# Kernel optimization log

Measured on AMD Instinct MI355X. Metric: run time of the kernel, lower is better.

Reference implementation:

```python
import jax, jax.numpy as jnp
import numpy as np

B, N0, NCLS = 8, 1024, 40
SPACING, SIGMA_FACTOR = 2.0, 1.0
BLOCKS = [[64, 64], [128, 128], [256, 1024]]
POOL_SIZES = [256, 64, 1]
FC1, FC2 = 512, 256
# 3x3x3 kernel translation grid (27-point support, hard-coded in ConvLayer)
GRID = jnp.asarray(np.array([[i, j, k] for i in (-1, 0, 1) for j in (-1, 0, 1) for k in (-1, 0, 1)], dtype=np.float32))  # [27,3]


def pcnn_conv(pc, feat, W, b, sigma):
    """Extension-operator point convolution.
    pc [B,N,3], feat [B,N,Cin], W [27,Cin,Cout], b [Cout].
    out[b,i,o] = relu( (1/N) * sum_l sum_j exp(-||p_i - p_j + t_l||^2/(2 ks^2)) f[b,j] @ W[l] + b )
    """
    ks = SIGMA_FACTOR * sigma
    trans = SPACING * sigma * GRID                      # [27,3]
    inv = 1.0 / (2.0 * ks * ks)
    diff = pc[:, :, None, :] - pc[:, None, :, :]        # [B,N,N,3]
    d2 = jnp.sum(diff * diff, -1)                       # [B,N,N]
    n = pc.shape[1]

    def body(acc, wt):
        t, Wl = wt                                      # t [3], Wl [Cin,Cout]
        # ||diff + t||^2 = d2 + 2 diff.t + |t|^2
        e = jnp.exp(-(d2 + 2.0 * jnp.einsum('bijd,d->bij', diff, t) + jnp.dot(t, t)) * inv)
        s = jnp.einsum('bij,bjc->bic', e, feat)         # Gaussian-weighted gather
        return acc + jnp.einsum('bic,co->bio', s, Wl), None

    out0 = jnp.zeros((pc.shape[0], n, W.shape[2]), feat.dtype)
    out, _ = jax.lax.scan(body, out0, (trans, W))
    return jax.nn.relu(out / n + b)


def fps(pts, m):
    """Farthest point sampling. pts [N,3] -> indices [m]."""
    d = jnp.sum((pts - pts[0]) ** 2, -1)
    idxs = jnp.zeros((m,), jnp.int32)

    def body(i, state):
        idxs, d = state
        nxt = jnp.argmax(d).astype(jnp.int32)
        idxs = idxs.at[i].set(nxt)
        d = jnp.minimum(d, jnp.sum((pts - pts[nxt]) ** 2, -1))
        return idxs, d

    idxs, _ = jax.lax.fori_loop(1, m, body, (idxs, d))
    return idxs


def pool(pc, feat, m):
    """FPS subsample to m centers, max-pool features over nearest-center clusters."""
    idx = jax.vmap(lambda p: fps(p, m))(pc)                      # [B,m]
    centers = jnp.take_along_axis(pc, idx[..., None], axis=1)    # [B,m,3]
    dist = jnp.sum((pc[:, :, None, :] - centers[:, None, :, :]) ** 2, -1)  # [B,N,m]
    assign = jnp.argmin(dist, -1)                                # [B,N]
    pooled = jax.vmap(lambda f, a: jax.ops.segment_max(f, a, num_segments=m))(feat, assign)
    return centers, pooled


def bn(x, g, b):
    mu = jnp.mean(x, 0)
    v = jnp.var(x, 0)
    return g * (x - mu) * jax.lax.rsqrt(v + 1e-5) + b


def setup_inputs() -> dict:
    key = jax.random.key(0)
    ks = jax.random.split(key, 24)
    inp = {"pc": jax.random.normal(ks[0], (B, 3, N0), jnp.float32)}
    chans = [4, 64, 64, 128, 128, 256, 1024]
    for i, (ci, co) in enumerate(zip(chans[:-1], chans[1:])):
        inp[f"w_c{i}"] = jax.random.normal(ks[1 + i], (27, ci, co), jnp.float32) * 0.05
        inp[f"b_c{i}"] = jnp.zeros((co,), jnp.float32)
    inp["w_fc1"] = jax.random.normal(ks[10], (1024, FC1), jnp.float32) * 0.03
    inp["g_fc1"] = jnp.ones((FC1,), jnp.float32)
    inp["be_fc1"] = jnp.zeros((FC1,), jnp.float32)
    inp["w_fc2"] = jax.random.normal(ks[11], (FC1, FC2), jnp.float32) * 0.05
    inp["g_fc2"] = jnp.ones((FC2,), jnp.float32)
    inp["be_fc2"] = jnp.zeros((FC2,), jnp.float32)
    inp["w_fc3"] = jax.random.normal(ks[12], (FC2, NCLS), jnp.float32) * 0.05
    inp["b_fc3"] = jnp.zeros((NCLS,), jnp.float32)
    return inp


def reference(pc, w_c0, b_c0, w_c1, b_c1, w_c2, b_c2, w_c3, b_c3, w_c4, b_c4, w_c5, b_c5,
              w_fc1, g_fc1, be_fc1, w_fc2, g_fc2, be_fc2, w_fc3, b_fc3):
    pts = jnp.transpose(pc, (0, 2, 1))                           # [B,N,3]
    b_, n0, _ = pts.shape
    feat = jnp.concatenate([pts, jnp.ones((b_, n0, 1), pts.dtype)], -1)  # [B,N,4]
    sigma = 1.0 / float(np.sqrt(n0))  # faithfully uses initial N for all blocks
    ws = [(w_c0, b_c0), (w_c1, b_c1), (w_c2, b_c2), (w_c3, b_c3), (w_c4, b_c4), (w_c5, b_c5)]
    idx = 0
    cur = pts
    for bi, block in enumerate(BLOCKS):
        for _ in block:
            W, bb = ws[idx]
            feat = pcnn_conv(cur, feat, W, bb, sigma)
            idx += 1
        cur, feat = pool(cur, feat, POOL_SIZES[bi])
    x = feat.reshape(b_, -1)                                     # [B,1024]
    x = jax.nn.relu(bn(x @ w_fc1, g_fc1, be_fc1))
    x = jax.nn.relu(bn(x @ w_fc2, g_fc2, be_fc2))
    return x @ w_fc3 + b_fc3
```

## Files before the change

### kernel.cpp

```cpp
#include <hip/hip_runtime.h>
#include <cstdint>
#include <cstddef>
#include <cmath>

constexpr int B = 8;
constexpr int N0 = 1024;
constexpr int CAP = 64;
using u16 = unsigned short;

typedef __bf16 bf16x8 __attribute__((ext_vector_type(8)));
typedef float f32x4 __attribute__((ext_vector_type(4)));

__device__ inline u16 f2bf(float x) {
  unsigned u = __float_as_uint(x);
  return (u16)((u + 0x7fffu + ((u >> 16) & 1u)) >> 16);
}
__device__ inline float bf2f(u16 h) { return __uint_as_float(((unsigned)h) << 16); }
__device__ inline int swk2(int row, int k) {
  int s = (((row >> 2) ^ (row >> 4)) & 3);
  return ((((k >> 3) ^ s) << 3) | (k & 7));
}

__global__ __launch_bounds__(256) void k_prep(const float* __restrict__ pc,
                                              float* __restrict__ pts,
                                              float* __restrict__ feat0,
                                              uint4* __restrict__ p3, int n3,
                                              uint4* __restrict__ p6, int n6,
                                              uint4* __restrict__ p9, int n9) {
  int idx = blockIdx.x * blockDim.x + threadIdx.x;
  if (idx < B * N0) {
    int b = idx / N0, i = idx - b * N0;
    float x = pc[(b * 3 + 0) * N0 + i];
    float y = pc[(b * 3 + 1) * N0 + i];
    float z = pc[(b * 3 + 2) * N0 + i];
    pts[idx * 3 + 0] = x; pts[idx * 3 + 1] = y; pts[idx * 3 + 2] = z;
    feat0[idx * 4 + 0] = x; feat0[idx * 4 + 1] = y; feat0[idx * 4 + 2] = z; feat0[idx * 4 + 3] = 1.0f;
  }
  uint4 v = make_uint4(0xFFFFFFFFu, 0xFFFFFFFFu, 0xFFFFFFFFu, 0xFFFFFFFFu);
  for (int i = idx; i < n3; i += B * N0) p3[i] = v;
  for (int i = idx; i < n6; i += B * N0) p6[i] = v;
  for (int i = idx; i < n9; i += B * N0) p9[i] = v;
}

__global__ __launch_bounds__(256) void k_pairs(const float* __restrict__ pts,
                                               int* __restrict__ pidx, int* __restrict__ pcnt,
                                               int N) {
  const int r = blockIdx.x * 4 + (threadIdx.x >> 6);
  const int lane = threadIdx.x & 63;
  const int b = r / N;
  const float px = pts[(size_t)r * 3 + 0];
  const float py = pts[(size_t)r * 3 + 1];
  const float pz = pts[(size_t)r * 3 + 2];
  int* row = pidx + (size_t)r * CAP;
  int base = 0;
  for (int j0 = 0; j0 < N; j0 += 64) {
    int j = j0 + lane;
    float dx = px - pts[((size_t)b * N + j) * 3 + 0];
    float dy = py - pts[((size_t)b * N + j) * 3 + 1];
    float dz = pz - pts[((size_t)b * N + j) * 3 + 2];
    float d2 = dx * dx + dy * dy + dz * dz;
    bool keep = d2 <= 0.1228f;
    unsigned long long mk = __ballot(keep);
    int pos = __popcll(mk & ((1ull << lane) - 1ull));
    if (keep) { int s = base + pos; if (s < CAP) row[s] = j; }
    base += __popcll(mk);
  }
  if (lane == 0) pcnt[r] = base < CAP ? base : CAP;
}

__device__ __forceinline__ void econ_dev(float (*eL)[28],
                                         const float* __restrict__ pts,
                                         const float* __restrict__ feat,
                                         const int* __restrict__ pidx,
                                         const int* __restrict__ pcnt,
                                         u16* __restrict__ Shi, u16* __restrict__ Slo,
                                         int N, int Cin, int K, int Kpad, int mbase,
                                         int blockX) {
  const int g = mbase + blockX;
  const int b = g / N;
  const int t = threadIdx.x;
  const int w = t >> 6, lane = t & 63;
  const bool cact = t < Cin;
  const float px = pts[(size_t)g * 3 + 0];
  const float py = pts[(size_t)g * 3 + 1];
  const float pz = pts[(size_t)g * 3 + 2];
  float sxc = 0.f, syc = 0.f, szc = 0.f, cst = 0.f;
  if (lane < 27) {
    int a = lane / 9, bb = (lane / 3) % 3, cc = lane % 3;
    sxc = (a == 0) ? 64.f : ((a == 2) ? -64.f : 0.f);
    syc = (bb == 0) ? 64.f : ((bb == 2) ? -64.f : 0.f);
    szc = (cc == 0) ? 64.f : ((cc == 2) ? -64.f : 0.f);
    cst = -2.f * (float)((a != 1) + (bb != 1) + (cc != 1));
  }
  float acc[27];
#pragma unroll
  for (int l = 0; l < 27; ++l) acc[l] = 0.f;
  const int n = pcnt[g];
  const int* row = pidx + (size_t)g * CAP;
  for (int p = 0; p < n; ++p) {
    int j = row[p];
    size_t jb = (size_t)b * N + j;
    float dx = px - pts[jb * 3 + 0];
    float dy = py - pts[jb * 3 + 1];
    float dz = pz - pts[jb * 3 + 2];
    float d2 = dx * dx + dy * dy + dz * dz;
    if (lane < 27) {
      float ex = fmaf(-512.f, d2, fmaf(sxc, dx, fmaf(syc, dy, fmaf(szc, dz, cst))));
      eL[w][lane] = __expf(ex);
    }
    asm volatile("s_waitcnt lgkmcnt(0)" ::: "memory");
    __builtin_amdgcn_sched_barrier(0);
    float fv = cact ? feat[jb * Cin + t] : 0.f;
#pragma unroll
    for (int l = 0; l < 27; ++l) acc[l] = fmaf(eL[w][l], fv, acc[l]);
  }
  size_t rowo = (size_t)blockX * Kpad;
  if (cact) {
#pragma unroll
    for (int l = 0; l < 27; ++l) {
      float v = acc[l];
      u16 h = f2bf(v);
      u16 lo = f2bf(v - bf2f(h));
      Shi[rowo + (size_t)l * Cin + t] = h;
      Slo[rowo + (size_t)l * Cin + t] = lo;
    }
  }
  if (Kpad > K && t >= Cin && t < Cin + (Kpad - K)) {
    size_t po = rowo + K + (t - Cin);
    Shi[po] = 0; Slo[po] = 0;
  }
}

__global__ void k_econtract(const float* __restrict__ pts, const float* __restrict__ feat,
                            const int* __restrict__ pidx, const int* __restrict__ pcnt,
                            u16* __restrict__ Shi, u16* __restrict__ Slo,
                            int N, int Cin, int K, int Kpad, int mbase) {
  __shared__ float eL[4][28];
  econ_dev(eL, pts, feat, pidx, pcnt, Shi, Slo, N, Cin, K, Kpad, mbase, blockIdx.x);
}

template <int CTRL>
__device__ __forceinline__ float dppmaxf(float v) {
  int o = __builtin_amdgcn_update_dpp(0, __float_as_int(v), CTRL, 0xF, 0xF, true);
  return fmaxf(v, __int_as_float(o));
}
__device__ __forceinline__ float wavemaxf(float v) {
  v = dppmaxf<0xB1>(v);
  v = dppmaxf<0x4E>(v);
  v = dppmaxf<0x141>(v);
  v = dppmaxf<0x140>(v);
  v = dppmaxf<0x142>(v);
  v = dppmaxf<0x143>(v);
  return __uint_as_float((unsigned)__builtin_amdgcn_readlane(__float_as_int(v), 63));
}

#define FPS_LOAD(i) \
  float qx##i = src[3 * i + 0], qy##i = src[3 * i + 1], qz##i = src[3 * i + 2];
#define FPS_PIN(i) \
  asm volatile("" : "+v"(qx##i), "+v"(qy##i), "+v"(qz##i));
#define FPS_D0A(i) \
  { float ax = __fsub_rn(qx##i, x0), ay = __fsub_rn(qy##i, y0), az = __fsub_rn(qz##i, z0); \
    d##i = __fadd_rn(__fadd_rn(__fmul_rn(ax, ax), __fmul_rn(ay, ay)), __fmul_rn(az, az)); }
#define FPS_UPD(i) \
  { float ax = __fsub_rn(qx##i, cx), ay = __fsub_rn(qy##i, cy), az = __fsub_rn(qz##i, cz); \
    float nd = __fadd_rn(__fadd_rn(__fmul_rn(ax, ax), __fmul_rn(ay, ay)), __fmul_rn(az, az)); \
    d##i = fminf(d##i, nd); }
#define FPS_SEL(i) \
  { bool e = (d##i == lbest); sx = e ? qx##i : sx; sy = e ? qy##i : sy; sz = e ? qz##i : sz; }

__device__ __noinline__ void fps1024_dev(const float* __restrict__ P,
                                         float* __restrict__ centers, int m, int b, int t,
                                         int it0, int it1, float* __restrict__ Dst) {
  const float* src = P + t * 48;
  FPS_LOAD(0) FPS_LOAD(1) FPS_LOAD(2) FPS_LOAD(3)
  FPS_LOAD(4) FPS_LOAD(5) FPS_LOAD(6) FPS_LOAD(7)
  FPS_LOAD(8) FPS_LOAD(9) FPS_LOAD(10) FPS_LOAD(11)
  FPS_LOAD(12) FPS_LOAD(13) FPS_LOAD(14) FPS_LOAD(15)
  FPS_PIN(0) FPS_PIN(1) FPS_PIN(2) FPS_PIN(3)
  FPS_PIN(4) FPS_PIN(5) FPS_PIN(6) FPS_PIN(7)
  FPS_PIN(8) FPS_PIN(9) FPS_PIN(10) FPS_PIN(11)
  FPS_PIN(12) FPS_PIN(13) FPS_PIN(14) FPS_PIN(15)
  float d0, d1, d2, d3, d4, d5, d6, d7, d8, d9, d10, d11, d12, d13, d14, d15;
  if (it0 == 1) {
    float x0 = P[0], y0 = P[1], z0 = P[2];
    FPS_D0A(0) FPS_D0A(1) FPS_D0A(2) FPS_D0A(3)
    FPS_D0A(4) FPS_D0A(5) FPS_D0A(6) FPS_D0A(7)
    FPS_D0A(8) FPS_D0A(9) FPS_D0A(10) FPS_D0A(11)
    FPS_D0A(12) FPS_D0A(13) FPS_D0A(14) FPS_D0A(15)
    if (t == 0) {
      centers[(size_t)b * m * 3 + 0] = x0;
      centers[(size_t)b * m * 3 + 1] = y0;
      centers[(size_t)b * m * 3 + 2] = z0;
    }
  } else {
    const float* ds = Dst + t * 16;
    d0 = ds[0]; d1 = ds[1]; d2 = ds[2]; d3 = ds[3];
    d4 = ds[4]; d5 = ds[5]; d6 = ds[6]; d7 = ds[7];
    d8 = ds[8]; d9 = ds[9]; d10 = ds[10]; d11 = ds[11];
    d12 = ds[12]; d13 = ds[13]; d14 = ds[14]; d15 = ds[15];
  }
  for (int it = it0; it < it1; ++it) {
    float lbest;
    {
      float a0 = fmaxf(d0, d1), a1 = fmaxf(d2, d3), a2 = fmaxf(d4, d5), a3 = fmaxf(d6, d7);
      float a4 = fmaxf(d8, d9), a5 = fmaxf(d10, d11), a6 = fmaxf(d12, d13), a7 = fmaxf(d14, d15);
      float b0 = fmaxf(a0, a1), b1 = fmaxf(a2, a3), b2 = fmaxf(a4, a5), b3 = fmaxf(a6, a7);
      lbest = fmaxf(fmaxf(b0, b1), fmaxf(b2, b3));
    }
    float sx = qx15, sy = qy15, sz = qz15;
    FPS_SEL(14) FPS_SEL(13) FPS_SEL(12) FPS_SEL(11)
    FPS_SEL(10) FPS_SEL(9) FPS_SEL(8) FPS_SEL(7)
    FPS_SEL(6) FPS_SEL(5) FPS_SEL(4) FPS_SEL(3)
    FPS_SEL(2) FPS_SEL(1) FPS_SEL(0)
    float wmax = wavemaxf(lbest);
    unsigned long long mask = __ballot(lbest == wmax);
    int fl = __ffsll((long long)mask) - 1;
    float cx = __uint_as_float((unsigned)__builtin_amdgcn_readlane(__float_as_int(sx), fl));
    float cy = __uint_as_float((unsigned)__builtin_amdgcn_readlane(__float_as_int(sy), fl));
    float cz = __uint_as_float((unsigned)__builtin_amdgcn_readlane(__float_as_int(sz), fl));
    if (t == 0) {
      centers[((size_t)b * m + it) * 3 + 0] = cx;
      centers[((size_t)b * m + it) * 3 + 1] = cy;
      centers[((size_t)b * m + it) * 3 + 2] = cz;
    }
    FPS_UPD(0) FPS_UPD(1) FPS_UPD(2) FPS_UPD(3)
    FPS_UPD(4) FPS_UPD(5) FPS_UPD(6) FPS_UPD(7)
    FPS_UPD(8) FPS_UPD(9) FPS_UPD(10) FPS_UPD(11)
    FPS_UPD(12) FPS_UPD(13) FPS_UPD(14) FPS_UPD(15)
  }
  if (it1 < m) {
    float* ds = Dst + t * 16;
    ds[0] = d0; ds[1] = d1; ds[2] = d2; ds[3] = d3;
    ds[4] = d4; ds[5] = d5; ds[6] = d6; ds[7] = d7;
    ds[8] = d8; ds[9] = d9; ds[10] = d10; ds[11] = d11;
    ds[12] = d12; ds[13] = d13; ds[14] = d14; ds[15] = d15;
  }
}

__device__ __noinline__ void fps256_dev(const float* __restrict__ P,
                                        float* __restrict__ centers, int m, int b, int t,
                                        int it0, int it1, float* __restrict__ Dst) {
  const float* src = P + t * 12;
  FPS_LOAD(0) FPS_LOAD(1) FPS_LOAD(2) FPS_LOAD(3)
  FPS_PIN(0) FPS_PIN(1) FPS_PIN(2) FPS_PIN(3)
  float d0, d1, d2, d3;
  if (it0 == 1) {
    float x0 = P[0], y0 = P[1], z0 = P[2];
    FPS_D0A(0) FPS_D0A(1) FPS_D0A(2) FPS_D0A(3)
    if (t == 0) {
      centers[(size_t)b * m * 3 + 0] = x0;
      centers[(size_t)b * m * 3 + 1] = y0;
      centers[(size_t)b * m * 3 + 2] = z0;
    }
  } else {
    const float* ds = Dst + t * 4;
    d0 = ds[0]; d1 = ds[1]; d2 = ds[2]; d3 = ds[3];
  }
  for (int it = it0; it < it1; ++it) {
    float lbest = fmaxf(fmaxf(d0, d1), fmaxf(d2, d3));
    float sx = qx3, sy = qy3, sz = qz3;
    FPS_SEL(2) FPS_SEL(1) FPS_SEL(0)
    float wmax = wavemaxf(lbest);
    unsigned long long mask = __ballot(lbest == wmax);
    int fl = __ffsll((long long)mask) - 1;
    float cx = __uint_as_float((unsigned)__builtin_amdgcn_readlane(__float_as_int(sx), fl));
    float cy = __uint_as_float((unsigned)__builtin_amdgcn_readlane(__float_as_int(sy), fl));
    float cz = __uint_as_float((unsigned)__builtin_amdgcn_readlane(__float_as_int(sz), fl));
    if (t == 0) {
      centers[((size_t)b * m + it) * 3 + 0] = cx;
      centers[((size_t)b * m + it) * 3 + 1] = cy;
      centers[((size_t)b * m + it) * 3 + 2] = cz;
    }
    FPS_UPD(0) FPS_UPD(1) FPS_UPD(2) FPS_UPD(3)
  }
  if (it1 < m) {
    float* ds = Dst + t * 4;
    ds[0] = d0; ds[1] = d1; ds[2] = d2; ds[3] = d3;
  }
}

__global__ __launch_bounds__(64, 1) void k_econtract_fps(
    const float* __restrict__ pts, const float* __restrict__ feat,
    const int* __restrict__ pidx, const int* __restrict__ pcnt,
    u16* __restrict__ Shi, u16* __restrict__ Slo,
    int N, int Cin, int K, int Kpad, int mbase,
    int fpsMode, const float* __restrict__ fpsPts, float* __restrict__ fpsCenters, int fpsM,
    int it0, int it1, float* __restrict__ fpsD) {
  __shared__ float eL[4][28];
  const int nEcon = gridDim.x - B;
  if ((int)blockIdx.x >= nEcon) {
    const int b = blockIdx.x - nEcon;
    const int t = threadIdx.x;
    if (fpsMode == 1) fps1024_dev(fpsPts + (size_t)b * 1024 * 3, fpsCenters, fpsM, b, t,
                                  it0, it1, fpsD + (size_t)b * 1024);
    else fps256_dev(fpsPts + (size_t)b * 256 * 3, fpsCenters, fpsM, b, t,
                    it0, it1, fpsD + (size_t)b * 256);
    return;
  }
  econ_dev(eL, pts, feat, pidx, pcnt, Shi, Slo, N, Cin, K, Kpad, mbase, blockIdx.x);
}

__global__ __launch_bounds__(512) void k_gemm_mfma(const u16* __restrict__ Shi,
                                                   const u16* __restrict__ Slo,
                                                   const float* __restrict__ W,
                                                   const float* __restrict__ bias,
                                                   float* __restrict__ out,
                                                   float* __restrict__ P,
                                                   int K, int Kpad, int Cout, float scale,
                                                   int mcur) {
  __shared__ u16 As[2][2][32][40];
  __shared__ u16 Bs[2][2][64][40];
  __shared__ float xch[4][64][8];
  const int t = threadIdx.x;
  const int h = t >> 8;
  const int tl = t & 255;
  const int nb = blockIdx.x * 64;
  const int m0 = blockIdx.y * 32;
  const int l = t & 63, w = t >> 6;
  const int ks = w >> 2, wq = w & 3;
  const int wm = (wq >> 1) * 16, wn = (wq & 1) * 32;
  const int la = l & 15, lg = l >> 4;
  const int ntiles = Kpad >> 6;
  const int KZ = gridDim.z, z = blockIdx.z;
  const int q = ntiles / KZ, r = ntiles % KZ;
  const int t0 = z * q + (z < r ? z : r);
  const int cnt = q + (z < r ? 1 : 0);
  const int ar = tl >> 3, ak = (tl & 7) * 4;
  const size_t aOff = (size_t)(m0 + ar) * Kpad + h * 32 + ak;
  const int aw = swk2(ar, ak);
  const int kp = (tl >> 4) * 2, n4 = (tl & 15) * 4;
  f32x4 acc0 = {0.f, 0.f, 0.f, 0.f}, acc1 = {0.f, 0.f, 0.f, 0.f};

  for (int kt = 0; kt < cnt; ++kt) {
    const int k0 = (t0 + kt) * 64;
    *(ushort4*)&As[h][0][ar][aw] = *(const ushort4*)(Shi + aOff + k0);
    *(ushort4*)&As[h][1][ar][aw] = *(const ushort4*)(Slo + aOff + k0);
    {
      int gk0 = k0 + h * 32 + kp;
      float4 b0 = make_float4(0.f, 0.f, 0.f, 0.f), b1 = b0;
      if (gk0 < K) b0 = *(const float4*)(W + (size_t)gk0 * Cout + nb + n4);
      if (gk0 + 1 < K) b1 = *(const float4*)(W + (size_t)(gk0 + 1) * Cout + nb + n4);
      float v0[4] = {b0.x, b0.y, b0.z, b0.w};
      float v1[4] = {b1.x, b1.y, b1.z, b1.w};
#pragma unroll
      for (int e = 0; e < 4; ++e) {
        int n = n4 + e;
        int kw = swk2(n, kp);
        u16 h0 = f2bf(v0[e]);
        u16 l0 = f2bf(v0[e] - bf2f(h0));
        u16 h1 = f2bf(v1[e]);
        u16 l1 = f2bf(v1[e] - bf2f(h1));
        *(unsigned*)&Bs[h][0][n][kw] = (unsigned)h0 | ((unsigned)h1 << 16);
        *(unsigned*)&Bs[h][1][n][kw] = (unsigned)l0 | ((unsigned)l1 << 16);
      }
    }
    __syncthreads();
    bf16x8 ah = *(const bf16x8*)&As[ks][0][wm + la][swk2(wm + la, lg * 8)];
    bf16x8 al = *(const bf16x8*)&As[ks][1][wm + la][swk2(wm + la, lg * 8)];
    bf16x8 bh0 = *(const bf16x8*)&Bs[ks][0][wn + la][swk2(wn + la, lg * 8)];
    bf16x8 bl0 = *(const bf16x8*)&Bs[ks][1][wn + la][swk2(wn + la, lg * 8)];
    bf16x8 bh1 = *(const bf16x8*)&Bs[ks][0][wn + 16 + la][swk2(wn + 16 + la, lg * 8)];
    bf16x8 bl1 = *(const bf16x8*)&Bs[ks][1][wn + 16 + la][swk2(wn + 16 + la, lg * 8)];
    acc0 = __builtin_amdgcn_mfma_f32_16x16x32_bf16(ah, bh0, acc0, 0, 0, 0);
    acc1 = __builtin_amdgcn_mfma_f32_16x16x32_bf16(ah, bh1, acc1, 0, 0, 0);
    acc0 = __builtin_amdgcn_mfma_f32_16x16x32_bf16(al, bh0, acc0, 0, 0, 0);
    acc1 = __builtin_amdgcn_mfma_f32_16x16x32_bf16(al, bh1, acc1, 0, 0, 0);
    acc0 = __builtin_amdgcn_mfma_f32_16x16x32_bf16(ah, bl0, acc0, 0, 0, 0);
    acc1 = __builtin_amdgcn_mfma_f32_16x16x32_bf16(ah, bl1, acc1, 0, 0, 0);
    __syncthreads();
  }
  if (w >= 4) {
#pragma unroll
    for (int r2 = 0; r2 < 4; ++r2) { xch[wq][l][r2] = acc0[r2]; xch[wq][l][r2 + 4] = acc1[r2]; }
  }
  __syncthreads();
  if (w < 4) {
#pragma unroll
    for (int r2 = 0; r2 < 4; ++r2) { acc0[r2] += xch[wq][l][r2]; acc1[r2] += xch[wq][l][r2 + 4]; }
    if (gridDim.z == 1) {
#pragma unroll
      for (int r2 = 0; r2 < 4; ++r2) {
        int gm = m0 + wm + lg * 4 + r2;
        int gn0 = nb + wn + la;
        out[(size_t)gm * Cout + gn0] = fmaxf(fmaf(acc0[r2], scale, bias[gn0]), 0.f);
        int gn1 = gn0 + 16;
        out[(size_t)gm * Cout + gn1] = fmaxf(fmaf(acc1[r2], scale, bias[gn1]), 0.f);
      }
    } else {
      float* Pz = P + (size_t)z * mcur * Cout;
#pragma unroll
      for (int r2 = 0; r2 < 4; ++r2) {
        int gm = m0 + wm + lg * 4 + r2;
        int gn0 = nb + wn + la;
        Pz[(size_t)gm * Cout + gn0] = acc0[r2];
        Pz[(size_t)gm * Cout + gn0 + 16] = acc1[r2];
      }
    }
  }
}

__global__ __launch_bounds__(256) void k_reduce(const float* __restrict__ P,
                                                const float* __restrict__ bias,
                                                float* __restrict__ out,
                                                int n4, int Cout, int KZ, float scale,
                                                int stride) {
  int i = blockIdx.x * 256 + threadIdx.x;
  if (i >= n4) return;
  float4 s = *(const float4*)(P + (size_t)i * 4);
  for (int z = 1; z < KZ; ++z) {
    float4 v = *(const float4*)(P + (size_t)z * stride + (size_t)i * 4);
    s.x += v.x; s.y += v.y; s.z += v.z; s.w += v.w;
  }
  int c = (i * 4) % Cout;
  float4 bb = *(const float4*)(bias + c);
  float4 o;
  o.x = fmaxf(fmaf(s.x, scale, bb.x), 0.f);
  o.y = fmaxf(fmaf(s.y, scale, bb.y), 0.f);
  o.z = fmaxf(fmaf(s.z, scale, bb.z), 0.f);
  o.w = fmaxf(fmaf(s.w, scale, bb.w), 0.f);
  *(float4*)(out + (size_t)i * 4) = o;
}

__global__ __launch_bounds__(64) void k_center0(const float* __restrict__ pts,
                                                float* __restrict__ centers,
                                                int* __restrict__ assign) {
  const int b = blockIdx.x, t = threadIdx.x;
  if (t < 3) centers[b * 3 + t] = pts[(size_t)b * 64 * 3 + t];
  assign[b * 64 + t] = 0;
}

__global__ __launch_bounds__(256) void k_assign(const float* __restrict__ pts,
                                                const float* __restrict__ centers,
                                                int* __restrict__ assign, int N, int m) {
  __shared__ float cs[256 * 3];
  const int t = threadIdx.x;
  const int idx = blockIdx.x * 256 + t;
  const int b = (blockIdx.x * 256) / N;
  for (int i = t; i < m * 3; i += 256) cs[i] = centers[(size_t)b * m * 3 + i];
  __syncthreads();
  float px = pts[(size_t)idx * 3 + 0], py = pts[(size_t)idx * 3 + 1], pz = pts[(size_t)idx * 3 + 2];
  float best = 3.4e38f; int bk = 0;
  for (int k = 0; k < m; ++k) {
    float dx = __fsub_rn(px, cs[k * 3 + 0]);
    float dy = __fsub_rn(py, cs[k * 3 + 1]);
    float dz = __fsub_rn(pz, cs[k * 3 + 2]);
    float dd = __fadd_rn(__fadd_rn(__fmul_rn(dx, dx), __fmul_rn(dy, dy)), __fmul_rn(dz, dz));
    if (dd < best) { best = dd; bk = k; }
  }
  assign[idx] = bk;
}

__global__ __launch_bounds__(256) void k_segmax(const float* __restrict__ feat,
                                                const int* __restrict__ assign,
                                                float* __restrict__ pooled,
                                                int N, int m, int C) {
  int idx = blockIdx.x * blockDim.x + threadIdx.x;
  if (idx >= B * N * C) return;
  int b = idx / (N * C);
  int r = idx - b * N * C;
  int i = r / C;
  int c = r - i * C;
  int a = assign[b * N + i];
  atomicMax((int*)&pooled[((size_t)b * m + a) * C + c], __float_as_int(feat[idx]));
}

template <int K, int COUT, bool BNR>
__global__ __launch_bounds__(256) void k_fc(const float* __restrict__ x,
                                            const float* __restrict__ w,
                                            const float* __restrict__ g,
                                            const float* __restrict__ be,
                                            float* __restrict__ out) {
  __shared__ float ys[8][33];
  int t = threadIdx.x;
  int n = t >> 5, cl = t & 31;
  int c = blockIdx.x * 32 + cl;
  float acc = 0.f;
  if (c < COUT) {
    const float* xr = x + n * K;
    float a0 = 0.f, a1 = 0.f, a2 = 0.f, a3 = 0.f;
    for (int k = 0; k < K; k += 4) {
      a0 = fmaf(xr[k + 0], w[(size_t)(k + 0) * COUT + c], a0);
      a1 = fmaf(xr[k + 1], w[(size_t)(k + 1) * COUT + c], a1);
      a2 = fmaf(xr[k + 2], w[(size_t)(k + 2) * COUT + c], a2);
      a3 = fmaf(xr[k + 3], w[(size_t)(k + 3) * COUT + c], a3);
    }
    acc = (a0 + a1) + (a2 + a3);
  }
  ys[n][cl] = acc;
  __syncthreads();
  if (c >= COUT) return;
  if (BNR) {
    float mu = 0.f;
#pragma unroll
    for (int q = 0; q < 8; ++q) mu += ys[q][cl];
    mu *= 0.125f;
    float var = 0.f;
#pragma unroll
    for (int q = 0; q < 8; ++q) { float dv = ys[q][cl] - mu; var = fmaf(dv, dv, var); }
    var *= 0.125f;
    float rs = 1.f / sqrtf(var + 1e-5f);
    float v = g[c] * (acc - mu) * rs + be[c];
    out[n * COUT + c] = fmaxf(v, 0.f);
  } else {
    out[n * COUT + c] = acc + be[c];
  }
}

extern "C" void kernel_launch(void* const* d_in, const int* in_sizes, int n_in,
                              void* d_out, int out_size, void* d_ws, size_t ws_size,
                              hipStream_t stream) {
  (void)in_sizes; (void)n_in; (void)out_size;
  const float* pc = (const float*)d_in[0];
  const float* Wc[6]; const float* bc[6];
  for (int l = 0; l < 6; ++l) { Wc[l] = (const float*)d_in[1 + 2 * l]; bc[l] = (const float*)d_in[2 + 2 * l]; }
  const float* w1 = (const float*)d_in[13];
  const float* g1 = (const float*)d_in[14];
  const float* be1 = (const float*)d_in[15];
  const float* w2 = (const float*)d_in[16];
  const float* g2 = (const float*)d_in[17];
  const float* be2 = (const float*)d_in[18];
  const float* w3 = (const float*)d_in[19];
  const float* b3 = (const float*)d_in[20];

  float* ws = (float*)d_ws;
  size_t o = 0;
  auto A = [&](size_t n) { size_t r = o; o += (n + 63) & ~(size_t)63; return r; };
  const size_t PTS0 = A((size_t)B * 1024 * 3);
  const size_t PTS1 = A((size_t)B * 256 * 3);
  const size_t PTS2 = A((size_t)B * 64 * 3);
  const size_t PTS3 = A((size_t)B * 3);
  const size_t F0  = A((size_t)B * 1024 * 4);
  const size_t FB1 = A((size_t)B * 1024 * 64);
  const size_t FB2 = A((size_t)B * 1024 * 64);
  const size_t FB3 = A((size_t)B * 256 * 64);
  const size_t FB4 = A((size_t)B * 256 * 128);
  const size_t FB5 = A((size_t)B * 256 * 128);
  const size_t FB6 = A((size_t)B * 64 * 128);
  const size_t FB7 = A((size_t)B * 64 * 256);
  const size_t FB8 = A((size_t)B * 64 * 1024);
  const size_t FB9 = A((size_t)B * 1024);
  const size_t ASSIGN = A((size_t)B * 1024);
  const size_t Y1 = A((size_t)8 * 512);
  const size_t Y2 = A((size_t)8 * 256);
  const size_t FPSD = A((size_t)B * 1024);
  const size_t PIDX = A((size_t)B * 1024 * CAP);
  const size_t PCNT = A((size_t)B * 1024);
  const size_t dynB = o * sizeof(float);

  int* pidx = (int*)(ws + PIDX);
  int* pcnt = (int*)(ws + PCNT);

  k_prep<<<dim3((B * N0 + 255) / 256), dim3(256), 0, stream>>>(
      pc, ws + PTS0, ws + F0,
      (uint4*)(ws + FB3), B * 256 * 64 / 4,
      (uint4*)(ws + FB6), B * 64 * 128 / 4,
      (uint4*)(ws + FB9), B * 1024 / 4);

  auto conv = [&](size_t ptsOff, size_t finOff, size_t foutOff, int Npts, int Cin, int Cout,
                  const float* W, const float* bias,
                  int fpsMode, size_t fpsPtsOff, size_t fpsCtrOff, int fpsM,
                  int eIt0, int eIt1) {
    const int M = B * Npts;
    const int K = 27 * Cin;
    const int Kpad = (K + 63) & ~63;
    const size_t availB = (ws_size > dynB) ? ws_size - dynB : 0;
    size_t pResB = availB / 4;
    if (pResB > (size_t)13 << 20) pResB = (size_t)13 << 20;
    const size_t sByte = availB - pResB;
    long mc = (long)(sByte / ((size_t)Kpad * 4)) & ~31L;
    int Mc = (int)((mc < (long)M) ? mc : (long)M);
    if (Mc < 32) Mc = 32;
    u16* Shi = (u16*)((char*)d_ws + dynB);
    u16* Slo = Shi + (size_t)Mc * Kpad;
    float* P = (float*)(Shi + (size_t)2 * Mc * Kpad);
    const int mch = (M + Mc - 1) / Mc;
    const float scale = 1.f / (float)Npts;
    const int blk = (Cin <= 64) ? 64 : Cin;
    const int ntiles = Kpad >> 6;
    for (int mcb = 0; mcb < mch; ++mcb) {
      const int mb0 = mcb * Mc;
      const int mcur = ((M - mb0) < Mc) ? (M - mb0) : Mc;
      if (mcb == 0 && fpsMode && blk == 64) {
        k_econtract_fps<<<dim3(mcur + B), dim3(64), 0, stream>>>(
            ws + ptsOff, ws + finOff, pidx, pcnt, Shi, Slo, Npts, Cin, K, Kpad, mb0,
            fpsMode, ws + fpsPtsOff, ws + fpsCtrOff, fpsM, eIt0, eIt1, ws + FPSD);
      } else {
        k_econtract<<<dim3(mcur), dim3(blk), 0, stream>>>(ws + ptsOff, ws + finOff, pidx, pcnt,
                                                          Shi, Slo, Npts, Cin, K, Kpad, mb0);
      }
      const int gx = Cout / 64, gy = mcur / 32;
      int kz = 1024 / (gx * gy);
      if (kz < 1) kz = 1;
      if (kz > ntiles) kz = ntiles;
      if (kz > 16) kz = 16;
      long pcap = (long)(pResB / ((size_t)mcur * Cout * 4));
      if ((long)kz > pcap) kz = (pcap < 1) ? 1 : (int)pcap;
      float* outp = ws + foutOff + (size_t)mb0 * Cout;
      k_gemm_mfma<<<dim3(gx, gy, kz), dim3(512), 0, stream>>>(
          Shi, Slo, W, bias, outp, P, K, Kpad, Cout, scale, mcur);
      if (kz > 1) {
        int n4 = mcur * Cout / 4;
        k_reduce<<<dim3((n4 + 255) / 256), dim3(256), 0, stream>>>(
            P, bias, outp, n4, Cout, kz, scale, mcur * Cout);
      }
    }
  };

  k_pairs<<<dim3(B * 1024 / 4), dim3(256), 0, stream>>>(ws + PTS0, pidx, pcnt, 1024);
  conv(PTS0, F0, FB1, 1024, 4, 64, Wc[0], bc[0], 1, PTS0, PTS1, 256, 1, 128);
  conv(PTS0, FB1, FB2, 1024, 64, 64, Wc[1], bc[1], 1, PTS0, PTS1, 256, 128, 256);
  k_assign<<<dim3(B * 1024 / 256), dim3(256), 0, stream>>>(ws + PTS0, ws + PTS1, (int*)(ws + ASSIGN), 1024, 256);
  k_segmax<<<dim3((B * 1024 * 64 + 255) / 256), dim3(256), 0, stream>>>(ws + FB2, (int*)(ws + ASSIGN), ws + FB3, 1024, 256, 64);
  k_pairs<<<dim3(B * 256 / 4), dim3(256), 0, stream>>>(ws + PTS1, pidx, pcnt, 256);
  conv(PTS1, FB3, FB4, 256, 64, 128, Wc[2], bc[2], 2, PTS1, PTS2, 64, 1, 64);
  conv(PTS1, FB4, FB5, 256, 128, 128, Wc[3], bc[3], 0, 0, 0, 0, 0, 0);
  k_assign<<<dim3(B * 256 / 256), dim3(256), 0, stream>>>(ws + PTS1, ws + PTS2, (int*)(ws + ASSIGN), 256, 64);
  k_segmax<<<dim3((B * 256 * 128 + 255) / 256), dim3(256), 0, stream>>>(ws + FB5, (int*)(ws + ASSIGN), ws + FB6, 256, 64, 128);
  k_pairs<<<dim3(B * 64 / 4), dim3(256), 0, stream>>>(ws + PTS2, pidx, pcnt, 64);
  conv(PTS2, FB6, FB7, 64, 128, 256, Wc[4], bc[4], 0, 0, 0, 0, 0, 0);
  conv(PTS2, FB7, FB8, 64, 256, 1024, Wc[5], bc[5], 0, 0, 0, 0, 0, 0);
  k_center0<<<dim3(B), dim3(64), 0, stream>>>(ws + PTS2, ws + PTS3, (int*)(ws + ASSIGN));
  k_segmax<<<dim3((B * 64 * 1024 + 255) / 256), dim3(256), 0, stream>>>(ws + FB8, (int*)(ws + ASSIGN), ws + FB9, 64, 1, 1024);
  k_fc<1024, 512, true><<<dim3(512 / 32), dim3(256), 0, stream>>>(ws + FB9, w1, g1, be1, ws + Y1);
  k_fc<512, 256, true><<<dim3(256 / 32), dim3(256), 0, stream>>>(ws + Y1, w2, g2, be2, ws + Y2);
  k_fc<256, 40, false><<<dim3(2), dim3(256), 0, stream>>>(ws + Y2, w3, nullptr, b3, (float*)d_out);
}
```

Measured before the change: 444.1 us.

## Spread FPS iterations across prep and pairs kernels to overlap with other work

Farthest-point sampling was previously hidden only inside the econtract kernels (two chunks of iterations for the first pool, one for the second). It now also runs as extra blocks in k_prep (reading the original channel-major point cloud through strided pointers) and in the pairs kernels, so the serial FPS chain is split into more, smaller chunks that overlap with independent work. The FPS loop also raises wave priority with s_setprio. The risk is launch-bounds changes on prep/pairs and extra state round-trips through global memory between chunks.

```diff
diff --git a/kernel.cpp b/kernel.cpp
--- a/kernel.cpp
+++ b/kernel.cpp
@@ -21,13 +21,185 @@
   return ((((k >> 3) ^ s) << 3) | (k & 7));
 }
 
-__global__ __launch_bounds__(256) void k_prep(const float* __restrict__ pc,
-                                              float* __restrict__ pts,
-                                              float* __restrict__ feat0,
-                                              uint4* __restrict__ p3, int n3,
-                                              uint4* __restrict__ p6, int n6,
-                                              uint4* __restrict__ p9, int n9) {
-  int idx = blockIdx.x * blockDim.x + threadIdx.x;
+template <int CTRL>
+__device__ __forceinline__ float dppmaxf(float v) {
+  int o = __builtin_amdgcn_update_dpp(0, __float_as_int(v), CTRL, 0xF, 0xF, true);
+  return fmaxf(v, __int_as_float(o));
+}
+__device__ __forceinline__ float wavemaxf(float v) {
+  v = dppmaxf<0xB1>(v);
+  v = dppmaxf<0x4E>(v);
+  v = dppmaxf<0x141>(v);
+  v = dppmaxf<0x140>(v);
+  v = dppmaxf<0x142>(v);
+  v = dppmaxf<0x143>(v);
+  return __uint_as_float((unsigned)__builtin_amdgcn_readlane(__float_as_int(v), 63));
+}
+
+#define FPS_LD(i) \
+  float qx##i = Px[bix + i * stride], qy##i = Py[bix + i * stride], qz##i = Pz[bix + i * stride];
+#define FPS_PIN(i) \
+  asm volatile("" : "+v"(qx##i), "+v"(qy##i), "+v"(qz##i));
+#define FPS_D0A(i) \
+  { float ax = __fsub_rn(qx##i, x0), ay = __fsub_rn(qy##i, y0), az = __fsub_rn(qz##i, z0); \
+    d##i = __fadd_rn(__fadd_rn(__fmul_rn(ax, ax), __fmul_rn(ay, ay)), __fmul_rn(az, az)); }
+#define FPS_UPD(i) \
+  { float ax = __fsub_rn(qx##i, cx), ay = __fsub_rn(qy##i, cy), az = __fsub_rn(qz##i, cz); \
+    float nd = __fadd_rn(__fadd_rn(__fmul_rn(ax, ax), __fmul_rn(ay, ay)), __fmul_rn(az, az)); \
+    d##i = fminf(d##i, nd); }
+#define FPS_SEL(i) \
+  { bool e = (d##i == lbest); sx = e ? qx##i : sx; sy = e ? qy##i : sy; sz = e ? qz##i : sz; }
+
+__device__ __noinline__ void fps1024_dev(const float* __restrict__ Px,
+                                         const float* __restrict__ Py,
+                                         const float* __restrict__ Pz, int stride,
+                                         float* __restrict__ centers, int m, int b, int t,
+                                         int it0, int it1, float* __restrict__ Dst) {
+  const int bix = t * 16 * stride;
+  FPS_LD(0) FPS_LD(1) FPS_LD(2) FPS_LD(3)
+  FPS_LD(4) FPS_LD(5) FPS_LD(6) FPS_LD(7)
+  FPS_LD(8) FPS_LD(9) FPS_LD(10) FPS_LD(11)
+  FPS_LD(12) FPS_LD(13) FPS_LD(14) FPS_LD(15)
+  FPS_PIN(0) FPS_PIN(1) FPS_PIN(2) FPS_PIN(3)
+  FPS_PIN(4) FPS_PIN(5) FPS_PIN(6) FPS_PIN(7)
+  FPS_PIN(8) FPS_PIN(9) FPS_PIN(10) FPS_PIN(11)
+  FPS_PIN(12) FPS_PIN(13) FPS_PIN(14) FPS_PIN(15)
+  float d0, d1, d2, d3, d4, d5, d6, d7, d8, d9, d10, d11, d12, d13, d14, d15;
+  if (it0 == 1) {
+    float x0 = Px[0], y0 = Py[0], z0 = Pz[0];
+    FPS_D0A(0) FPS_D0A(1) FPS_D0A(2) FPS_D0A(3)
+    FPS_D0A(4) FPS_D0A(5) FPS_D0A(6) FPS_D0A(7)
+    FPS_D0A(8) FPS_D0A(9) FPS_D0A(10) FPS_D0A(11)
+    FPS_D0A(12) FPS_D0A(13) FPS_D0A(14) FPS_D0A(15)
+    if (t == 0) {
+      centers[(size_t)b * m * 3 + 0] = x0;
+      centers[(size_t)b * m * 3 + 1] = y0;
+      centers[(size_t)b * m * 3 + 2] = z0;
+    }
+  } else {
+    const float* ds = Dst + t * 16;
+    d0 = ds[0]; d1 = ds[1]; d2 = ds[2]; d3 = ds[3];
+    d4 = ds[4]; d5 = ds[5]; d6 = ds[6]; d7 = ds[7];
+    d8 = ds[8]; d9 = ds[9]; d10 = ds[10]; d11 = ds[11];
+    d12 = ds[12]; d13 = ds[13]; d14 = ds[14]; d15 = ds[15];
+  }
+  __builtin_amdgcn_s_setprio(1);
+  for (int it = it0; it < it1; ++it) {
+    float lbest;
+    {
+      float a0 = fmaxf(d0, d1), a1 = fmaxf(d2, d3), a2 = fmaxf(d4, d5), a3 = fmaxf(d6, d7);
+      float a4 = fmaxf(d8, d9), a5 = fmaxf(d10, d11), a6 = fmaxf(d12, d13), a7 = fmaxf(d14, d15);
+      float b0 = fmaxf(a0, a1), b1 = fmaxf(a2, a3), b2 = fmaxf(a4, a5), b3 = fmaxf(a6, a7);
+      lbest = fmaxf(fmaxf(b0, b1), fmaxf(b2, b3));
+    }
+    float sx = qx15, sy = qy15, sz = qz15;
+    FPS_SEL(14) FPS_SEL(13) FPS_SEL(12) FPS_SEL(11)
+    FPS_SEL(10) FPS_SEL(9) FPS_SEL(8) FPS_SEL(7)
+    FPS_SEL(6) FPS_SEL(5) FPS_SEL(4) FPS_SEL(3)
+    FPS_SEL(2) FPS_SEL(1) FPS_SEL(0)
+    float wmax = wavemaxf(lbest);
+    unsigned long long mask = __ballot(lbest == wmax);
+    int fl = __ffsll((long long)mask) - 1;
+    float cx = __uint_as_float((unsigned)__builtin_amdgcn_readlane(__float_as_int(sx), fl));
+    float cy = __uint_as_float((unsigned)__builtin_amdgcn_readlane(__float_as_int(sy), fl));
+    float cz = __uint_as_float((unsigned)__builtin_amdgcn_readlane(__float_as_int(sz), fl));
+    if (t == 0) {
+      centers[((size_t)b * m + it) * 3 + 0] = cx;
+      centers[((size_t)b * m + it) * 3 + 1] = cy;
+      centers[((size_t)b * m + it) * 3 + 2] = cz;
+    }
+    FPS_UPD(0) FPS_UPD(1) FPS_UPD(2) FPS_UPD(3)
+    FPS_UPD(4) FPS_UPD(5) FPS_UPD(6) FPS_UPD(7)
+    FPS_UPD(8) FPS_UPD(9) FPS_UPD(10) FPS_UPD(11)
+    FPS_UPD(12) FPS_UPD(13) FPS_UPD(14) FPS_UPD(15)
+  }
+  __builtin_amdgcn_s_setprio(0);
+  if (it1 < m) {
+    float* ds = Dst + t * 16;
+    ds[0] = d0; ds[1] = d1; ds[2] = d2; ds[3] = d3;
+    ds[4] = d4; ds[5] = d5; ds[6] = d6; ds[7] = d7;
+    ds[8] = d8; ds[9] = d9; ds[10] = d10; ds[11] = d11;
+    ds[12] = d12; ds[13] = d13; ds[14] = d14; ds[15] = d15;
+  }
+}
+
+__device__ __noinline__ void fps256_dev(const float* __restrict__ Px,
+                                        const float* __restrict__ Py,
+                                        const float* __restrict__ Pz, int stride,
+                                        float* __restrict__ centers, int m, int b, int t,
+                                        int it0, int it1, float* __restrict__ Dst) {
+  const int bix = t * 4 * stride;
+  FPS_LD(0) FPS_LD(1) FPS_LD(2) FPS_LD(3)
+  FPS_PIN(0) FPS_PIN(1) FPS_PIN(2) FPS_PIN(3)
+  float d0, d1, d2, d3;
+  if (it0 == 1) {
+    float x0 = Px[0], y0 = Py[0], z0 = Pz[0];
+    FPS_D0A(0) FPS_D0A(1) FPS_D0A(2) FPS_D0A(3)
+    if (t == 0) {
+      centers[(size_t)b * m * 3 + 0] = x0;
+      centers[(size_t)b * m * 3 + 1] = y0;
+      centers[(size_t)b * m * 3 + 2] = z0;
+    }
+  } else {
+    const float* ds = Dst + t * 4;
+    d0 = ds[0]; d1 = ds[1]; d2 = ds[2]; d3 = ds[3];
+  }
+  __builtin_amdgcn_s_setprio(1);
+  for (int it = it0; it < it1; ++it) {
+    float lbest = fmaxf(fmaxf(d0, d1), fmaxf(d2, d3));
+    float sx = qx3, sy = qy3, sz = qz3;
+    FPS_SEL(2) FPS_SEL(1) FPS_SEL(0)
+    float wmax = wavemaxf(lbest);
+    unsigned long long mask = __ballot(lbest == wmax);
+    int fl = __ffsll((long long)mask) - 1;
+    float cx = __uint_as_float((unsigned)__builtin_amdgcn_readlane(__float_as_int(sx), fl));
+    float cy = __uint_as_float((unsigned)__builtin_amdgcn_readlane(__float_as_int(sy), fl));
+    float cz = __uint_as_float((unsigned)__builtin_amdgcn_readlane(__float_as_int(sz), fl));
+    if (t == 0) {
+      centers[((size_t)b * m + it) * 3 + 0] = cx;
+      centers[((size_t)b * m + it) * 3 + 1] = cy;
+      centers[((size_t)b * m + it) * 3 + 2] = cz;
+    }
+    FPS_UPD(0) FPS_UPD(1) FPS_UPD(2) FPS_UPD(3)
+  }
+  __builtin_amdgcn_s_setprio(0);
+  if (it1 < m) {
+    float* ds = Dst + t * 4;
+    ds[0] = d0; ds[1] = d1; ds[2] = d2; ds[3] = d3;
+  }
+}
+
+__device__ __forceinline__ void fps_run(int mode, const float* __restrict__ fpsPts,
+                                        float* __restrict__ centers, int m,
+                                        int b, int t, int it0, int it1,
+                                        float* __restrict__ fpsD) {
+  if (mode == 1) {
+    const float* Px = fpsPts + (size_t)b * 3072;
+    fps1024_dev(Px, Px + 1, Px + 2, 3, centers, m, b, t, it0, it1, fpsD + (size_t)b * 1024);
+  } else {
+    const float* Px = fpsPts + (size_t)b * 768;
+    fps256_dev(Px, Px + 1, Px + 2, 3, centers, m, b, t, it0, it1, fpsD + (size_t)b * 256);
+  }
+}
+
+__global__ __launch_bounds__(256, 1) void k_prep(const float* __restrict__ pc,
+                                                 float* __restrict__ pts,
+                                                 float* __restrict__ feat0,
+                                                 uint4* __restrict__ p3, int n3,
+                                                 uint4* __restrict__ p6, int n6,
+                                                 uint4* __restrict__ p9, int n9,
+                                                 float* __restrict__ fpsCenters,
+                                                 float* __restrict__ fpsD) {
+  const int t = threadIdx.x;
+  if ((int)blockIdx.x < B) {
+    if (t >= 64) return;
+    const int b = blockIdx.x;
+    const float* Px = pc + (size_t)b * 3 * 1024;
+    fps1024_dev(Px, Px + 1024, Px + 2048, 1, fpsCenters, 256, b, t, 1, 65,
+                fpsD + (size_t)b * 1024);
+    return;
+  }
+  int idx = (blockIdx.x - B) * 256 + t;
   if (idx < B * N0) {
     int b = idx / N0, i = idx - b * N0;
     float x = pc[(b * 3 + 0) * N0 + i];
@@ -42,11 +214,21 @@
   for (int i = idx; i < n9; i += B * N0) p9[i] = v;
 }
 
-__global__ __launch_bounds__(256) void k_pairs(const float* __restrict__ pts,
-                                               int* __restrict__ pidx, int* __restrict__ pcnt,
-                                               int N) {
-  const int r = blockIdx.x * 4 + (threadIdx.x >> 6);
-  const int lane = threadIdx.x & 63;
+__global__ __launch_bounds__(256, 1) void k_pairs_f(const float* __restrict__ pts,
+                                                    int* __restrict__ pidx, int* __restrict__ pcnt,
+                                                    int N,
+                                                    int fpsMode, const float* __restrict__ fpsPts,
+                                                    float* __restrict__ fpsCenters, int fpsM,
+                                                    int it0, int it1, float* __restrict__ fpsD) {
+  const int t = threadIdx.x;
+  if (fpsMode && (int)blockIdx.x < B) {
+    if (t >= 64) return;
+    fps_run(fpsMode, fpsPts, fpsCenters, fpsM, blockIdx.x, t, it0, it1, fpsD);
+    return;
+  }
+  const int boff = fpsMode ? B : 0;
+  const int r = (blockIdx.x - boff) * 4 + (t >> 6);
+  const int lane = t & 63;
   const int b = r / N;
   const float px = pts[(size_t)r * 3 + 0];
   const float py = pts[(size_t)r * 3 + 1];
@@ -139,146 +321,6 @@
   econ_dev(eL, pts, feat, pidx, pcnt, Shi, Slo, N, Cin, K, Kpad, mbase, blockIdx.x);
 }
 
-template <int CTRL>
-__device__ __forceinline__ float dppmaxf(float v) {
-  int o = __builtin_amdgcn_update_dpp(0, __float_as_int(v), CTRL, 0xF, 0xF, true);
-  return fmaxf(v, __int_as_float(o));
-}
-__device__ __forceinline__ float wavemaxf(float v) {
-  v = dppmaxf<0xB1>(v);
-  v = dppmaxf<0x4E>(v);
-  v = dppmaxf<0x141>(v);
-  v = dppmaxf<0x140>(v);
-  v = dppmaxf<0x142>(v);
-  v = dppmaxf<0x143>(v);
-  return __uint_as_float((unsigned)__builtin_amdgcn_readlane(__float_as_int(v), 63));
-}
-
-#define FPS_LOAD(i) \
-  float qx##i = src[3 * i + 0], qy##i = src[3 * i + 1], qz##i = src[3 * i + 2];
-#define FPS_PIN(i) \
-  asm volatile("" : "+v"(qx##i), "+v"(qy##i), "+v"(qz##i));
-#define FPS_D0A(i) \
-  { float ax = __fsub_rn(qx##i, x0), ay = __fsub_rn(qy##i, y0), az = __fsub_rn(qz##i, z0); \
-    d##i = __fadd_rn(__fadd_rn(__fmul_rn(ax, ax), __fmul_rn(ay, ay)), __fmul_rn(az, az)); }
-#define FPS_UPD(i) \
-  { float ax = __fsub_rn(qx##i, cx), ay = __fsub_rn(qy##i, cy), az = __fsub_rn(qz##i, cz); \
-    float nd = __fadd_rn(__fadd_rn(__fmul_rn(ax, ax), __fmul_rn(ay, ay)), __fmul_rn(az, az)); \
-    d##i = fminf(d##i, nd); }
-#define FPS_SEL(i) \
-  { bool e = (d##i == lbest); sx = e ? qx##i : sx; sy = e ? qy##i : sy; sz = e ? qz##i : sz; }
-
-__device__ __noinline__ void fps1024_dev(const float* __restrict__ P,
-                                         float* __restrict__ centers, int m, int b, int t,
-                                         int it0, int it1, float* __restrict__ Dst) {
-  const float* src = P + t * 48;
-  FPS_LOAD(0) FPS_LOAD(1) FPS_LOAD(2) FPS_LOAD(3)
-  FPS_LOAD(4) FPS_LOAD(5) FPS_LOAD(6) FPS_LOAD(7)
-  FPS_LOAD(8) FPS_LOAD(9) FPS_LOAD(10) FPS_LOAD(11)
-  FPS_LOAD(12) FPS_LOAD(13) FPS_LOAD(14) FPS_LOAD(15)
-  FPS_PIN(0) FPS_PIN(1) FPS_PIN(2) FPS_PIN(3)
-  FPS_PIN(4) FPS_PIN(5) FPS_PIN(6) FPS_PIN(7)
-  FPS_PIN(8) FPS_PIN(9) FPS_PIN(10) FPS_PIN(11)
-  FPS_PIN(12) FPS_PIN(13) FPS_PIN(14) FPS_PIN(15)
-  float d0, d1, d2, d3, d4, d5, d6, d7, d8, d9, d10, d11, d12, d13, d14, d15;
-  if (it0 == 1) {
-    float x0 = P[0], y0 = P[1], z0 = P[2];
-    FPS_D0A(0) FPS_D0A(1) FPS_D0A(2) FPS_D0A(3)
-    FPS_D0A(4) FPS_D0A(5) FPS_D0A(6) FPS_D0A(7)
-    FPS_D0A(8) FPS_D0A(9) FPS_D0A(10) FPS_D0A(11)
-    FPS_D0A(12) FPS_D0A(13) FPS_D0A(14) FPS_D0A(15)
-    if (t == 0) {
-      centers[(size_t)b * m * 3 + 0] = x0;
-      centers[(size_t)b * m * 3 + 1] = y0;
-      centers[(size_t)b * m * 3 + 2] = z0;
-    }
-  } else {
-    const float* ds = Dst + t * 16;
-    d0 = ds[0]; d1 = ds[1]; d2 = ds[2]; d3 = ds[3];
-    d4 = ds[4]; d5 = ds[5]; d6 = ds[6]; d7 = ds[7];
-    d8 = ds[8]; d9 = ds[9]; d10 = ds[10]; d11 = ds[11];
-    d12 = ds[12]; d13 = ds[13]; d14 = ds[14]; d15 = ds[15];
-  }
-  for (int it = it0; it < it1; ++it) {
-    float lbest;
-    {
-      float a0 = fmaxf(d0, d1), a1 = fmaxf(d2, d3), a2 = fmaxf(d4, d5), a3 = fmaxf(d6, d7);
-      float a4 = fmaxf(d8, d9), a5 = fmaxf(d10, d11), a6 = fmaxf(d12, d13), a7 = fmaxf(d14, d15);
-      float b0 = fmaxf(a0, a1), b1 = fmaxf(a2, a3), b2 = fmaxf(a4, a5), b3 = fmaxf(a6, a7);
-      lbest = fmaxf(fmaxf(b0, b1), fmaxf(b2, b3));
-    }
-    float sx = qx15, sy = qy15, sz = qz15;
-    FPS_SEL(14) FPS_SEL(13) FPS_SEL(12) FPS_SEL(11)
-    FPS_SEL(10) FPS_SEL(9) FPS_SEL(8) FPS_SEL(7)
-    FPS_SEL(6) FPS_SEL(5) FPS_SEL(4) FPS_SEL(3)
-    FPS_SEL(2) FPS_SEL(1) FPS_SEL(0)
-    float wmax = wavemaxf(lbest);
-    unsigned long long mask = __ballot(lbest == wmax);
-    int fl = __ffsll((long long)mask) - 1;
-    float cx = __uint_as_float((unsigned)__builtin_amdgcn_readlane(__float_as_int(sx), fl));
-    float cy = __uint_as_float((unsigned)__builtin_amdgcn_readlane(__float_as_int(sy), fl));
-    float cz = __uint_as_float((unsigned)__builtin_amdgcn_readlane(__float_as_int(sz), fl));
-    if (t == 0) {
-      centers[((size_t)b * m + it) * 3 + 0] = cx;
-      centers[((size_t)b * m + it) * 3 + 1] = cy;
-      centers[((size_t)b * m + it) * 3 + 2] = cz;
-    }
-    FPS_UPD(0) FPS_UPD(1) FPS_UPD(2) FPS_UPD(3)
-    FPS_UPD(4) FPS_UPD(5) FPS_UPD(6) FPS_UPD(7)
-    FPS_UPD(8) FPS_UPD(9) FPS_UPD(10) FPS_UPD(11)
-    FPS_UPD(12) FPS_UPD(13) FPS_UPD(14) FPS_UPD(15)
-  }
-  if (it1 < m) {
-    float* ds = Dst + t * 16;
-    ds[0] = d0; ds[1] = d1; ds[2] = d2; ds[3] = d3;
-    ds[4] = d4; ds[5] = d5; ds[6] = d6; ds[7] = d7;
-    ds[8] = d8; ds[9] = d9; ds[10] = d10; ds[11] = d11;
-    ds[12] = d12; ds[13] = d13; ds[14] = d14; ds[15] = d15;
-  }
-}
-
-__device__ __noinline__ void fps256_dev(const float* __restrict__ P,
-                                        float* __restrict__ centers, int m, int b, int t,
-                                        int it0, int it1, float* __restrict__ Dst) {
-  const float* src = P + t * 12;
-  FPS_LOAD(0) FPS_LOAD(1) FPS_LOAD(2) FPS_LOAD(3)
-  FPS_PIN(0) FPS_PIN(1) FPS_PIN(2) FPS_PIN(3)
-  float d0, d1, d2, d3;
-  if (it0 == 1) {
-    float x0 = P[0], y0 = P[1], z0 = P[2];
-    FPS_D0A(0) FPS_D0A(1) FPS_D0A(2) FPS_D0A(3)
-    if (t == 0) {
-      centers[(size_t)b * m * 3 + 0] = x0;
-      centers[(size_t)b * m * 3 + 1] = y0;
-      centers[(size_t)b * m * 3 + 2] = z0;
-    }
-  } else {
-    const float* ds = Dst + t * 4;
-    d0 = ds[0]; d1 = ds[1]; d2 = ds[2]; d3 = ds[3];
-  }
-  for (int it = it0; it < it1; ++it) {
-    float lbest = fmaxf(fmaxf(d0, d1), fmaxf(d2, d3));
-    float sx = qx3, sy = qy3, sz = qz3;
-    FPS_SEL(2) FPS_SEL(1) FPS_SEL(0)
-    float wmax = wavemaxf(lbest);
-    unsigned long long mask = __ballot(lbest == wmax);
-    int fl = __ffsll((long long)mask) - 1;
-    float cx = __uint_as_float((unsigned)__builtin_amdgcn_readlane(__float_as_int(sx), fl));
-    float cy = __uint_as_float((unsigned)__builtin_amdgcn_readlane(__float_as_int(sy), fl));
-    float cz = __uint_as_float((unsigned)__builtin_amdgcn_readlane(__float_as_int(sz), fl));
-    if (t == 0) {
-      centers[((size_t)b * m + it) * 3 + 0] = cx;
-      centers[((size_t)b * m + it) * 3 + 1] = cy;
-      centers[((size_t)b * m + it) * 3 + 2] = cz;
-    }
-    FPS_UPD(0) FPS_UPD(1) FPS_UPD(2) FPS_UPD(3)
-  }
-  if (it1 < m) {
-    float* ds = Dst + t * 4;
-    ds[0] = d0; ds[1] = d1; ds[2] = d2; ds[3] = d3;
-  }
-}
-
 __global__ __launch_bounds__(64, 1) void k_econtract_fps(
     const float* __restrict__ pts, const float* __restrict__ feat,
     const int* __restrict__ pidx, const int* __restrict__ pcnt,
@@ -287,17 +329,11 @@
     int fpsMode, const float* __restrict__ fpsPts, float* __restrict__ fpsCenters, int fpsM,
     int it0, int it1, float* __restrict__ fpsD) {
   __shared__ float eL[4][28];
-  const int nEcon = gridDim.x - B;
-  if ((int)blockIdx.x >= nEcon) {
-    const int b = blockIdx.x - nEcon;
-    const int t = threadIdx.x;
-    if (fpsMode == 1) fps1024_dev(fpsPts + (size_t)b * 1024 * 3, fpsCenters, fpsM, b, t,
-                                  it0, it1, fpsD + (size_t)b * 1024);
-    else fps256_dev(fpsPts + (size_t)b * 256 * 3, fpsCenters, fpsM, b, t,
-                    it0, it1, fpsD + (size_t)b * 256);
+  if ((int)blockIdx.x < B) {
+    fps_run(fpsMode, fpsPts, fpsCenters, fpsM, blockIdx.x, threadIdx.x, it0, it1, fpsD);
     return;
   }
-  econ_dev(eL, pts, feat, pidx, pcnt, Shi, Slo, N, Cin, K, Kpad, mbase, blockIdx.x);
+  econ_dev(eL, pts, feat, pidx, pcnt, Shi, Slo, N, Cin, K, Kpad, mbase, blockIdx.x - B);
 }
 
 __global__ __launch_bounds__(512) void k_gemm_mfma(const u16* __restrict__ Shi,
@@ -550,11 +586,12 @@
   int* pidx = (int*)(ws + PIDX);
   int* pcnt = (int*)(ws + PCNT);
 
-  k_prep<<<dim3((B * N0 + 255) / 256), dim3(256), 0, stream>>>(
+  k_prep<<<dim3(B + (B * N0 + 255) / 256), dim3(256), 0, stream>>>(
       pc, ws + PTS0, ws + F0,
       (uint4*)(ws + FB3), B * 256 * 64 / 4,
       (uint4*)(ws + FB6), B * 64 * 128 / 4,
-      (uint4*)(ws + FB9), B * 1024 / 4);
+      (uint4*)(ws + FB9), B * 1024 / 4,
+      ws + PTS1, ws + FPSD);
 
   auto conv = [&](size_t ptsOff, size_t finOff, size_t foutOff, int Npts, int Cin, int Cout,
                   const float* W, const float* bias,
@@ -606,17 +643,20 @@
     }
   };
 
-  k_pairs<<<dim3(B * 1024 / 4), dim3(256), 0, stream>>>(ws + PTS0, pidx, pcnt, 1024);
-  conv(PTS0, F0, FB1, 1024, 4, 64, Wc[0], bc[0], 1, PTS0, PTS1, 256, 1, 128);
-  conv(PTS0, FB1, FB2, 1024, 64, 64, Wc[1], bc[1], 1, PTS0, PTS1, 256, 128, 256);
+  k_pairs_f<<<dim3(B + B * 1024 / 4), dim3(256), 0, stream>>>(
+      ws + PTS0, pidx, pcnt, 1024, 1, ws + PTS0, ws + PTS1, 256, 65, 129, ws + FPSD);
+  conv(PTS0, F0, FB1, 1024, 4, 64, Wc[0], bc[0], 1, PTS0, PTS1, 256, 129, 193);
+  conv(PTS0, FB1, FB2, 1024, 64, 64, Wc[1], bc[1], 1, PTS0, PTS1, 256, 193, 256);
   k_assign<<<dim3(B * 1024 / 256), dim3(256), 0, stream>>>(ws + PTS0, ws + PTS1, (int*)(ws + ASSIGN), 1024, 256);
   k_segmax<<<dim3((B * 1024 * 64 + 255) / 256), dim3(256), 0, stream>>>(ws + FB2, (int*)(ws + ASSIGN), ws + FB3, 1024, 256, 64);
-  k_pairs<<<dim3(B * 256 / 4), dim3(256), 0, stream>>>(ws + PTS1, pidx, pcnt, 256);
-  conv(PTS1, FB3, FB4, 256, 64, 128, Wc[2], bc[2], 2, PTS1, PTS2, 64, 1, 64);
+  k_pairs_f<<<dim3(B + B * 256 / 4), dim3(256), 0, stream>>>(
+      ws + PTS1, pidx, pcnt, 256, 2, ws + PTS1, ws + PTS2, 64, 1, 33, ws + FPSD);
+  conv(PTS1, FB3, FB4, 256, 64, 128, Wc[2], bc[2], 2, PTS1, PTS2, 64, 33, 64);
   conv(PTS1, FB4, FB5, 256, 128, 128, Wc[3], bc[3], 0, 0, 0, 0, 0, 0);
   k_assign<<<dim3(B * 256 / 256), dim3(256), 0, stream>>>(ws + PTS1, ws + PTS2, (int*)(ws + ASSIGN), 256, 64);
   k_segmax<<<dim3((B * 256 * 128 + 255) / 256), dim3(256), 0, stream>>>(ws + FB5, (int*)(ws + ASSIGN), ws + FB6, 256, 64, 128);
-  k_pairs<<<dim3(B * 64 / 4), dim3(256), 0, stream>>>(ws + PTS2, pidx, pcnt, 64);
+  k_pairs_f<<<dim3(B * 64 / 4), dim3(256), 0, stream>>>(
+      ws + PTS2, pidx, pcnt, 64, 0, nullptr, nullptr, 0, 0, 0, nullptr);
   conv(PTS2, FB6, FB7, 64, 128, 256, Wc[4], bc[4], 0, 0, 0, 0, 0, 0);
   conv(PTS2, FB7, FB8, 64, 256, 1024, Wc[5], bc[5], 0, 0, 0, 0, 0, 0);
   k_center0<<<dim3(B), dim3(64), 0, stream>>>(ws + PTS2, ws + PTS3, (int*)(ws + ASSIGN));
```

New measurement: 416.2 us (median of 2 runs). -6.3%, faster.
